# Kernel optimization log

Measured on AMD Instinct MI355X. Metric: run time of the kernel, lower is better.

The kernel has to match this reference:

```python
import jax, jax.numpy as jnp
import numpy as np

N, P, Q, T, J, B, H = 262144, 64, 64, 2048, 512, 8, 64


def setup_inputs() -> dict:
    key = jax.random.key(0)
    ks = jax.random.split(key, 11)
    sH = 1.0 / np.sqrt(H).astype(np.float32)
    return {
        "idx": jax.random.randint(ks[0], (B,), 0, J),
        "seg_ids": jnp.sort(jax.random.randint(ks[1], (N,), 0, T)),
        "K": jax.random.normal(ks[2], (N, P), jnp.float32) * 0.1,
        "V": jax.random.normal(ks[3], (N, Q), jnp.float32),
        "S": jax.random.normal(ks[4], (P, J), jnp.float32) * 0.1,
        "W_ih": jax.random.normal(ks[5], (3 * H, Q), jnp.float32) * sH,
        "W_hh": jax.random.normal(ks[6], (3 * H, H), jnp.float32) * sH,
        "b_ih": jax.random.normal(ks[7], (3 * H,), jnp.float32) * sH,
        "b_hh": jax.random.normal(ks[8], (3 * H,), jnp.float32) * sH,
        "w_out": jax.random.normal(ks[9], (1, H), jnp.float32) * sH,
        "b_out": jax.random.normal(ks[10], (1,), jnp.float32) * sH,
    }


def reference(idx, seg_ids, K, V, S, W_ih, W_hh, b_ih, b_hh, w_out, b_out):
    # W[:, b] = K @ S[:, idx[b]]  -> [N, B]
    w = K @ S[:, idx]
    # ragged per-segment softmax over the N axis (segments = date windows)
    m = jax.ops.segment_max(w, seg_ids, num_segments=T)          # [T, B]
    e = jnp.exp(w - m[seg_ids])                                  # [N, B]
    denom = jax.ops.segment_sum(e, seg_ids, num_segments=T)     # [T, B]
    alpha = e / denom[seg_ids]                                   # [N, B]
    # weighted aggregation of V rows per segment: M[t, b] = sum_u alpha_u * V_u
    M = jax.ops.segment_sum(alpha[:, :, None] * V[:, None, :],
                            seg_ids, num_segments=T)             # [T, B, Q]
    X = jnp.transpose(M, (1, 0, 2))                              # [B, T, Q]

    # PyTorch GRU (gate order r,z,n). Faithful to the original bug: GRU was
    # built without batch_first=True, so axis 0 (B) is time, axis 1 (T) is batch.
    def step(h, x_t):  # x_t: [T, Q], h: [T, H]
        gi = x_t @ W_ih.T + b_ih                                 # [T, 3H]
        gh = h @ W_hh.T + b_hh                                   # [T, 3H]
        i_r, i_z, i_n = jnp.split(gi, 3, axis=1)
        h_r, h_z, h_n = jnp.split(gh, 3, axis=1)
        r = jax.nn.sigmoid(i_r + h_r)
        z = jax.nn.sigmoid(i_z + h_z)
        n = jnp.tanh(i_n + r * h_n)
        h_new = (1.0 - z) * n + z * h
        return h_new, h_new

    h0 = jnp.zeros((T, H), X.dtype)
    _, hs = jax.lax.scan(step, h0, X)                            # [B, T, H]
    preds = hs @ w_out.T + b_out                                 # [B, T, 1]
    return preds
```

## Files before the change

kernel.cpp:

```cpp
#include <hip/hip_runtime.h>
#include <math.h>

#define NN 262144
#define PP 64
#define QQ 64
#define TT 2048
#define JJ 512
#define BB 8
#define HH 64

__device__ __forceinline__ float lane_bcast(float v, int l) {
  return __int_as_float(__builtin_amdgcn_readlane(__float_as_int(v), l));
}

__global__ __launch_bounds__(256) void k_wp(const float* __restrict__ Kmat,
                                            const int* __restrict__ idx,
                                            const float* __restrict__ S,
                                            const int* __restrict__ seg_ids,
                                            float* __restrict__ ew,
                                            int* __restrict__ seg_start) {
  int tid = threadIdx.x;
  int gtid = blockIdx.x * 256 + tid;
  if (gtid <= TT) {
    int lo = 0, hi = NN;
    while (lo < hi) {
      int mid = (lo + hi) >> 1;
      if (seg_ids[mid] < gtid) lo = mid + 1; else hi = mid;
    }
    seg_start[gtid] = lo;
  }
  __shared__ __align__(16) float s_lds[BB * PP];
  for (int i = tid; i < BB * PP; i += 256) {
    int p = i >> 3, b = i & 7;
    s_lds[b * PP + p] = S[p * JJ + idx[b]];
  }
  __syncthreads();
  int n = blockIdx.x * 64 + (tid >> 2);
  int sub = tid & 3;
  const float4* Kp = reinterpret_cast<const float4*>(Kmat + (size_t)n * PP + sub * 16);
  float4 kq[4];
#pragma unroll
  for (int j = 0; j < 4; ++j) kq[j] = Kp[j];
  float acc[8];
#pragma unroll
  for (int b = 0; b < 8; ++b) acc[b] = 0.f;
#pragma unroll
  for (int j4 = 0; j4 < 4; ++j4) {
    float4 kk = kq[j4];
#pragma unroll
    for (int b = 0; b < 8; ++b) {
      const float4 sv = *reinterpret_cast<const float4*>(&s_lds[b * PP + sub * 16 + j4 * 4]);
      acc[b] += kk.x * sv.x + kk.y * sv.y + kk.z * sv.z + kk.w * sv.w;
    }
  }
#pragma unroll
  for (int b = 0; b < 8; ++b) {
    acc[b] += __shfl_xor(acc[b], 1);
    acc[b] += __shfl_xor(acc[b], 2);
  }
  float ox = (sub == 0) ? acc[0] : (sub == 1) ? acc[2] : (sub == 2) ? acc[4] : acc[6];
  float oy = (sub == 0) ? acc[1] : (sub == 1) ? acc[3] : (sub == 2) ? acc[5] : acc[7];
  reinterpret_cast<float2*>(ew + (size_t)n * 8)[sub] =
      make_float2(__expf(ox), __expf(oy));
}

__global__ __launch_bounds__(256) void k_segS(const float* __restrict__ ew,
                                              const float* __restrict__ V,
                                              const int* __restrict__ seg_start,
                                              float* __restrict__ M) {
  __shared__ __align__(16) float accred[4][8][64];
  __shared__ float reds[4][8];
  int tid = threadIdx.x;
  int t = blockIdx.x;
  int lane = tid & 63;
  int w = __builtin_amdgcn_readfirstlane(tid >> 6);
  int s = seg_start[t], e = seg_start[t + 1];
  int len = e - s;
  int chunk = (len + 3) >> 2;
  int b0 = __builtin_amdgcn_readfirstlane(s + w * chunk);
  int b1 = b0 + chunk; if (b1 > e) b1 = e;
  b1 = __builtin_amdgcn_readfirstlane(b1);
  if (b1 < b0) b1 = b0;

  float acc[8], se[8];
#pragma unroll
  for (int b = 0; b < 8; ++b) { acc[b] = 0.f; se[b] = 0.f; }

  int r = b0;
  for (; r + 4 <= b1; r += 4) {
#pragma unroll
    for (int u = 0; u < 4; ++u) {
      const float* er = ew + (size_t)(r + u) * 8;
      float e0 = er[0], e1 = er[1], e2 = er[2], e3 = er[3];
      float e4 = er[4], e5 = er[5], e6 = er[6], e7 = er[7];
      float v = V[(size_t)(r + u) * QQ + lane];
      acc[0] += e0 * v; acc[1] += e1 * v; acc[2] += e2 * v; acc[3] += e3 * v;
      acc[4] += e4 * v; acc[5] += e5 * v; acc[6] += e6 * v; acc[7] += e7 * v;
      se[0] += e0; se[1] += e1; se[2] += e2; se[3] += e3;
      se[4] += e4; se[5] += e5; se[6] += e6; se[7] += e7;
    }
  }
  for (; r < b1; ++r) {
    const float* er = ew + (size_t)r * 8;
    float e0 = er[0], e1 = er[1], e2 = er[2], e3 = er[3];
    float e4 = er[4], e5 = er[5], e6 = er[6], e7 = er[7];
    float v = V[(size_t)r * QQ + lane];
    acc[0] += e0 * v; acc[1] += e1 * v; acc[2] += e2 * v; acc[3] += e3 * v;
    acc[4] += e4 * v; acc[5] += e5 * v; acc[6] += e6 * v; acc[7] += e7 * v;
    se[0] += e0; se[1] += e1; se[2] += e2; se[3] += e3;
    se[4] += e4; se[5] += e5; se[6] += e6; se[7] += e7;
  }

#pragma unroll
  for (int b = 0; b < 8; ++b) accred[w][b][lane] = acc[b];
  if (lane == 0) {
#pragma unroll
    for (int b = 0; b < 8; ++b) reds[w][b] = se[b];
  }
  __syncthreads();
  for (int o = tid; o < 512; o += 256) {
    int b = o >> 6, q = o & 63;
    float dd = reds[0][b] + reds[1][b] + reds[2][b] + reds[3][b];
    float inv = (dd > 0.f) ? 1.f / dd : 0.f;
    float sum = accred[0][b][q] + accred[1][b][q] + accred[2][b][q] + accred[3][b][q];
    M[(size_t)t * 512 + o] = sum * inv;
  }
}

__global__ __launch_bounds__(256) void k_gi(const float* __restrict__ M,
                                            const float* __restrict__ W_ih,
                                            const float* __restrict__ b_ih,
                                            float* __restrict__ GI) {
  __shared__ float Wt[64 * 193];
  int tid = threadIdx.x;
  for (int i = tid; i < 192 * 64; i += 256) {
    int g = i >> 6, k = i & 63;
    Wt[k * 193 + g] = W_ih[i];
  }
  __syncthreads();
  int lane = tid & 63, wv = tid >> 6;
  int row0 = blockIdx.x * 32 + wv * 8;
  float x[8];
#pragma unroll
  for (int rr = 0; rr < 8; ++rr) {
    int rho = row0 + rr;
    int b = rho >> 11, t = rho & 2047;
    x[rr] = M[((size_t)t * 8 + b) * 64 + lane];
  }
  float bi0 = b_ih[lane], bi1 = b_ih[64 + lane], bi2 = b_ih[128 + lane];
  float a0[8], a1[8], a2[8];
#pragma unroll
  for (int rr = 0; rr < 8; ++rr) { a0[rr] = bi0; a1[rr] = bi1; a2[rr] = bi2; }
#pragma unroll
  for (int k = 0; k < 64; ++k) {
    float w0 = Wt[k * 193 + lane];
    float w1 = Wt[k * 193 + 64 + lane];
    float w2 = Wt[k * 193 + 128 + lane];
#pragma unroll
    for (int rr = 0; rr < 8; ++rr) {
      float xk = lane_bcast(x[rr], k);
      a0[rr] += w0 * xk; a1[rr] += w1 * xk; a2[rr] += w2 * xk;
    }
  }
#pragma unroll
  for (int rr = 0; rr < 8; ++rr) {
    size_t rho = (size_t)row0 + rr;
    GI[rho * 192 + lane]       = a0[rr];
    GI[rho * 192 + 64 + lane]  = a1[rr];
    GI[rho * 192 + 128 + lane] = a2[rr];
  }
}

__global__ __launch_bounds__(256) void k_gru(const float* __restrict__ GI,
                                             const float* __restrict__ W_hh,
                                             const float* __restrict__ b_hh,
                                             const float* __restrict__ w_out,
                                             const float* __restrict__ b_out,
                                             float* __restrict__ preds) {
  __shared__ __align__(16) float Wl[192 * 68];
  int tid = threadIdx.x;
  for (int i = tid; i < 192 * 16; i += 256) {
    int g = i >> 4, c = i & 15;
    *reinterpret_cast<float4*>(&Wl[g * 68 + c * 4]) =
        *reinterpret_cast<const float4*>(W_hh + g * 64 + c * 4);
  }
  __syncthreads();
  int lane = tid & 63, wv = tid >> 6;
  int t = blockIdx.x * 4 + wv;
  float bh0 = b_hh[lane], bh1 = b_hh[64 + lane], bh2 = b_hh[128 + lane];
  float wo = w_out[lane];
  float bo = b_out[0];
  const float* w0base = &Wl[lane * 68];
  const float* w1base = &Wl[(64 + lane) * 68];
  const float* w2base = &Wl[(128 + lane) * 68];

  float gr[8], gz[8], gn[8];
#pragma unroll
  for (int b = 0; b < 8; ++b) {
    size_t base = ((size_t)b * TT + t) * 192;
    gr[b] = GI[base + lane];
    gz[b] = GI[base + 64 + lane];
    gn[b] = GI[base + 128 + lane];
  }

  float h;
  {
    float r = 1.f / (1.f + __expf(-(gr[0] + bh0)));
    float z = 1.f / (1.f + __expf(-(gz[0] + bh1)));
    float nv = tanhf(gn[0] + r * bh2);
    h = (1.f - z) * nv;
    float pv = h * wo;
#pragma unroll
    for (int off = 32; off; off >>= 1) pv += __shfl_xor(pv, off);
    if (lane == 0) preds[t] = pv + bo;
  }
#pragma unroll
  for (int b = 1; b < 8; ++b) {
    float ar = bh0, az = bh1, an = bh2;
#pragma unroll
    for (int c = 0; c < 16; ++c) {
      const float4 w0 = *reinterpret_cast<const float4*>(w0base + c * 4);
      const float4 w1 = *reinterpret_cast<const float4*>(w1base + c * 4);
      const float4 w2 = *reinterpret_cast<const float4*>(w2base + c * 4);
      float a0 = lane_bcast(h, c * 4 + 0), a1 = lane_bcast(h, c * 4 + 1);
      float a2 = lane_bcast(h, c * 4 + 2), a3 = lane_bcast(h, c * 4 + 3);
      ar += w0.x * a0 + w0.y * a1 + w0.z * a2 + w0.w * a3;
      az += w1.x * a0 + w1.y * a1 + w1.z * a2 + w1.w * a3;
      an += w2.x * a0 + w2.y * a1 + w2.z * a2 + w2.w * a3;
    }
    float r = 1.f / (1.f + __expf(-(gr[b] + ar)));
    float z = 1.f / (1.f + __expf(-(gz[b] + az)));
    float nv = tanhf(gn[b] + r * an);
    h = (1.f - z) * nv + z * h;
    float pv = h * wo;
#pragma unroll
    for (int off = 32; off; off >>= 1) pv += __shfl_xor(pv, off);
    if (lane == 0) preds[(size_t)b * TT + t] = pv + bo;
  }
}

extern "C" void kernel_launch(void* const* d_in, const int* in_sizes, int n_in,
                              void* d_out, int out_size, void* d_ws, size_t ws_size,
                              hipStream_t stream) {
  const int*   idx     = (const int*)d_in[0];
  const int*   seg_ids = (const int*)d_in[1];
  const float* Kmat    = (const float*)d_in[2];
  const float* V       = (const float*)d_in[3];
  const float* S       = (const float*)d_in[4];
  const float* W_ih    = (const float*)d_in[5];
  const float* W_hh    = (const float*)d_in[6];
  const float* b_ih    = (const float*)d_in[7];
  const float* b_hh    = (const float*)d_in[8];
  const float* w_out   = (const float*)d_in[9];
  const float* b_out   = (const float*)d_in[10];
  float* out = (float*)d_out;

  char* ws = (char*)d_ws;
  int*   seg_start = (int*)(ws + 0);
  float* ew = (float*)(ws + 8448);
  float* M  = (float*)(ws + 8397056);
  float* GI = (float*)(ws + 12591360);

  hipLaunchKernelGGL(k_wp, dim3(NN / 64), dim3(256), 0, stream,
                     Kmat, idx, S, seg_ids, ew, seg_start);
  hipLaunchKernelGGL(k_segS, dim3(TT), dim3(256), 0, stream, ew, V, seg_start, M);
  hipLaunchKernelGGL(k_gi, dim3(512), dim3(256), 0, stream, M, W_ih, b_ih, GI);
  hipLaunchKernelGGL(k_gru, dim3(512), dim3(256), 0, stream, GI, W_hh, b_hh, w_out, b_out, out);
}
```

Before: 70.13 us.

## Fuse score kernel into segment aggregation, keeping exp weights in LDS

The matvec-plus-exp kernel and the per-segment weighted-sum kernel are merged into one kernel launched per segment. Each block binary-searches its own segment bounds, computes exp(K·S) for its rows into an LDS buffer, then accumulates the V rows from that buffer. This removes the global write and re-read of the N×8 exp-weight array and one launch. In exchange, the binary search runs in every block, threads sit idle when segments are short, and the LDS buffer holds at most 384 rows per segment, so a longer segment would be silently truncated.

```diff
diff --git a/kernel.cpp b/kernel.cpp
--- a/kernel.cpp
+++ b/kernel.cpp
@@ -13,74 +13,78 @@
   return __int_as_float(__builtin_amdgcn_readlane(__float_as_int(v), l));
 }
 
-__global__ __launch_bounds__(256) void k_wp(const float* __restrict__ Kmat,
-                                            const int* __restrict__ idx,
-                                            const float* __restrict__ S,
-                                            const int* __restrict__ seg_ids,
-                                            float* __restrict__ ew,
-                                            int* __restrict__ seg_start) {
+__global__ __launch_bounds__(256) void k_fusedS(const float* __restrict__ Kmat,
+                                                const int* __restrict__ idx,
+                                                const float* __restrict__ S,
+                                                const float* __restrict__ V,
+                                                const int* __restrict__ seg_ids,
+                                                float* __restrict__ M) {
+  __shared__ __align__(16) float s_cols[BB * PP];
+  __shared__ __align__(16) float ew_lds[384 * 8];
+  __shared__ __align__(16) float accred[4][8][64];
+  __shared__ float reds[4][8];
+  __shared__ int bounds[2];
   int tid = threadIdx.x;
-  int gtid = blockIdx.x * 256 + tid;
-  if (gtid <= TT) {
+  int t = blockIdx.x;
+  if (tid < 2) {
+    int target = t + tid;
     int lo = 0, hi = NN;
     while (lo < hi) {
       int mid = (lo + hi) >> 1;
-      if (seg_ids[mid] < gtid) lo = mid + 1; else hi = mid;
-    }
-    seg_start[gtid] = lo;
-  }
-  __shared__ __align__(16) float s_lds[BB * PP];
+      if (seg_ids[mid] < target) lo = mid + 1; else hi = mid;
+    }
+    bounds[tid] = lo;
+  }
   for (int i = tid; i < BB * PP; i += 256) {
     int p = i >> 3, b = i & 7;
-    s_lds[b * PP + p] = S[p * JJ + idx[b]];
-  }
-  __syncthreads();
-  int n = blockIdx.x * 64 + (tid >> 2);
-  int sub = tid & 3;
-  const float4* Kp = reinterpret_cast<const float4*>(Kmat + (size_t)n * PP + sub * 16);
-  float4 kq[4];
-#pragma unroll
-  for (int j = 0; j < 4; ++j) kq[j] = Kp[j];
-  float acc[8];
-#pragma unroll
-  for (int b = 0; b < 8; ++b) acc[b] = 0.f;
-#pragma unroll
-  for (int j4 = 0; j4 < 4; ++j4) {
-    float4 kk = kq[j4];
-#pragma unroll
-    for (int b = 0; b < 8; ++b) {
-      const float4 sv = *reinterpret_cast<const float4*>(&s_lds[b * PP + sub * 16 + j4 * 4]);
-      acc[b] += kk.x * sv.x + kk.y * sv.y + kk.z * sv.z + kk.w * sv.w;
-    }
-  }
-#pragma unroll
-  for (int b = 0; b < 8; ++b) {
-    acc[b] += __shfl_xor(acc[b], 1);
-    acc[b] += __shfl_xor(acc[b], 2);
-  }
-  float ox = (sub == 0) ? acc[0] : (sub == 1) ? acc[2] : (sub == 2) ? acc[4] : acc[6];
-  float oy = (sub == 0) ? acc[1] : (sub == 1) ? acc[3] : (sub == 2) ? acc[5] : acc[7];
-  reinterpret_cast<float2*>(ew + (size_t)n * 8)[sub] =
-      make_float2(__expf(ox), __expf(oy));
-}
-
-__global__ __launch_bounds__(256) void k_segS(const float* __restrict__ ew,
-                                              const float* __restrict__ V,
-                                              const int* __restrict__ seg_start,
-                                              float* __restrict__ M) {
-  __shared__ __align__(16) float accred[4][8][64];
-  __shared__ float reds[4][8];
-  int tid = threadIdx.x;
-  int t = blockIdx.x;
-  int lane = tid & 63;
-  int w = __builtin_amdgcn_readfirstlane(tid >> 6);
-  int s = seg_start[t], e = seg_start[t + 1];
+    s_cols[b * PP + p] = S[p * JJ + idx[b]];
+  }
+  __syncthreads();
+  int s = bounds[0], e = bounds[1];
+
+  {
+    int row_in = tid >> 2, sub = tid & 3;
+#pragma unroll
+    for (int pass = 0; pass < 6; ++pass) {
+      int base = s + (pass << 6);
+      if (base >= e) break;
+      int row = base + row_in;
+      if (row < e) {
+        const float4* Kp = reinterpret_cast<const float4*>(Kmat + (size_t)row * PP + sub * 16);
+        float4 kq[4];
+#pragma unroll
+        for (int j = 0; j < 4; ++j) kq[j] = Kp[j];
+        float a8[8];
+#pragma unroll
+        for (int b = 0; b < 8; ++b) a8[b] = 0.f;
+#pragma unroll
+        for (int j4 = 0; j4 < 4; ++j4) {
+          float4 kk = kq[j4];
+#pragma unroll
+          for (int b = 0; b < 8; ++b) {
+            const float4 sv = *reinterpret_cast<const float4*>(&s_cols[b * PP + sub * 16 + j4 * 4]);
+            a8[b] += kk.x * sv.x + kk.y * sv.y + kk.z * sv.z + kk.w * sv.w;
+          }
+        }
+#pragma unroll
+        for (int b = 0; b < 8; ++b) {
+          a8[b] += __shfl_xor(a8[b], 1);
+          a8[b] += __shfl_xor(a8[b], 2);
+        }
+        float ox = (sub == 0) ? a8[0] : (sub == 1) ? a8[2] : (sub == 2) ? a8[4] : a8[6];
+        float oy = (sub == 0) ? a8[1] : (sub == 1) ? a8[3] : (sub == 2) ? a8[5] : a8[7];
+        *reinterpret_cast<float2*>(&ew_lds[(row - s) * 8 + 2 * sub]) =
+            make_float2(__expf(ox), __expf(oy));
+      }
+    }
+  }
+  __syncthreads();
+
+  int lane = tid & 63, w = tid >> 6;
   int len = e - s;
   int chunk = (len + 3) >> 2;
-  int b0 = __builtin_amdgcn_readfirstlane(s + w * chunk);
-  int b1 = b0 + chunk; if (b1 > e) b1 = e;
-  b1 = __builtin_amdgcn_readfirstlane(b1);
-  if (b1 < b0) b1 = b0;
+  int b0 = s + w * chunk;
+  int b1 = b0 + chunk; if (b1 > e) b1 = e; if (b1 < b0) b1 = b0;
 
   float acc[8], se[8];
 #pragma unroll
@@ -90,25 +94,25 @@
   for (; r + 4 <= b1; r += 4) {
 #pragma unroll
     for (int u = 0; u < 4; ++u) {
-      const float* er = ew + (size_t)(r + u) * 8;
-      float e0 = er[0], e1 = er[1], e2 = er[2], e3 = er[3];
-      float e4 = er[4], e5 = er[5], e6 = er[6], e7 = er[7];
+      int ro = r + u - s;
+      float4 elo = *reinterpret_cast<const float4*>(&ew_lds[ro * 8]);
+      float4 ehi = *reinterpret_cast<const float4*>(&ew_lds[ro * 8 + 4]);
       float v = V[(size_t)(r + u) * QQ + lane];
-      acc[0] += e0 * v; acc[1] += e1 * v; acc[2] += e2 * v; acc[3] += e3 * v;
-      acc[4] += e4 * v; acc[5] += e5 * v; acc[6] += e6 * v; acc[7] += e7 * v;
-      se[0] += e0; se[1] += e1; se[2] += e2; se[3] += e3;
-      se[4] += e4; se[5] += e5; se[6] += e6; se[7] += e7;
+      acc[0] += elo.x * v; acc[1] += elo.y * v; acc[2] += elo.z * v; acc[3] += elo.w * v;
+      acc[4] += ehi.x * v; acc[5] += ehi.y * v; acc[6] += ehi.z * v; acc[7] += ehi.w * v;
+      se[0] += elo.x; se[1] += elo.y; se[2] += elo.z; se[3] += elo.w;
+      se[4] += ehi.x; se[5] += ehi.y; se[6] += ehi.z; se[7] += ehi.w;
     }
   }
   for (; r < b1; ++r) {
-    const float* er = ew + (size_t)r * 8;
-    float e0 = er[0], e1 = er[1], e2 = er[2], e3 = er[3];
-    float e4 = er[4], e5 = er[5], e6 = er[6], e7 = er[7];
+    int ro = r - s;
+    float4 elo = *reinterpret_cast<const float4*>(&ew_lds[ro * 8]);
+    float4 ehi = *reinterpret_cast<const float4*>(&ew_lds[ro * 8 + 4]);
     float v = V[(size_t)r * QQ + lane];
-    acc[0] += e0 * v; acc[1] += e1 * v; acc[2] += e2 * v; acc[3] += e3 * v;
-    acc[4] += e4 * v; acc[5] += e5 * v; acc[6] += e6 * v; acc[7] += e7 * v;
-    se[0] += e0; se[1] += e1; se[2] += e2; se[3] += e3;
-    se[4] += e4; se[5] += e5; se[6] += e6; se[7] += e7;
+    acc[0] += elo.x * v; acc[1] += elo.y * v; acc[2] += elo.z * v; acc[3] += elo.w * v;
+    acc[4] += ehi.x * v; acc[5] += ehi.y * v; acc[6] += ehi.z * v; acc[7] += ehi.w * v;
+    se[0] += elo.x; se[1] += elo.y; se[2] += elo.z; se[3] += elo.w;
+    se[4] += ehi.x; se[5] += ehi.y; se[6] += ehi.z; se[7] += ehi.w;
   }
 
 #pragma unroll
@@ -256,14 +260,11 @@
   float* out = (float*)d_out;
 
   char* ws = (char*)d_ws;
-  int*   seg_start = (int*)(ws + 0);
-  float* ew = (float*)(ws + 8448);
-  float* M  = (float*)(ws + 8397056);
-  float* GI = (float*)(ws + 12591360);
-
-  hipLaunchKernelGGL(k_wp, dim3(NN / 64), dim3(256), 0, stream,
-                     Kmat, idx, S, seg_ids, ew, seg_start);
-  hipLaunchKernelGGL(k_segS, dim3(TT), dim3(256), 0, stream, ew, V, seg_start, M);
+  float* M  = (float*)(ws + 0);
+  float* GI = (float*)(ws + 4194304);
+
+  hipLaunchKernelGGL(k_fusedS, dim3(TT), dim3(256), 0, stream,
+                     Kmat, idx, S, V, seg_ids, M);
   hipLaunchKernelGGL(k_gi, dim3(512), dim3(256), 0, stream, M, W_ih, b_ih, GI);
   hipLaunchKernelGGL(k_gru, dim3(512), dim3(256), 0, stream, GI, W_hh, b_hh, w_out, b_out, out);
 }
```

Result: no change. 70.19 us (+0.1%).
